# Performance work log

Measured on AMD Instinct MI355X. Metric: run time of the kernel, lower is better.

## Reference

```python
import jax, jax.numpy as jnp
import numpy as np

NB_EXPERTS = 16
TOP_K = 2


def setup_inputs() -> dict:
    key = jax.random.key(0)
    k1, k2, k3, k4, k5 = jax.random.split(key, 5)
    B, D, E, P = 8192, 768, NB_EXPERTS, 4
    return {
        "h": jax.random.normal(k1, (B, D, E), dtype=jnp.float32),
        "x": jax.random.normal(k2, (B, D), dtype=jnp.float32),
        "expert_weights": jax.random.normal(k3, (E, D), dtype=jnp.float32) * 0.02,
        "bias": jax.random.normal(k4, (E,), dtype=jnp.float32) * 0.02,
        "permutation_weights": jax.random.uniform(k5, (P, E, E), dtype=jnp.float32),
    }


def reference(h, x, expert_weights, bias, permutation_weights):
    # Router logits: [B, E]
    logits = x @ expert_weights.T + bias[None, :]
    # Top-k selection and scatter back to dense [B, E] (non-selected = 0)
    vals, idx = jax.lax.top_k(logits, TOP_K)
    B = logits.shape[0]
    rows = jnp.arange(B)[:, None]                       # [B, 1]
    scattered = jnp.zeros_like(logits).at[rows, idx].set(vals)
    # Mask zeros to -inf, softmax over experts (axis 1)
    masked = jnp.where(scattered == 0.0, -jnp.inf, scattered)
    softmaxes = jax.nn.softmax(masked, axis=1)          # [B, E]
    # Permutation: mean over leading axis, then bik,ij->bjk with k==1
    P_mean = jnp.mean(permutation_weights, axis=0)       # [E, E]
    s_perm = softmaxes @ P_mean                          # [B, E]
    # Weighted combine of expert outputs: [B, D, E] x [B, E] -> [B, D]
    y = jnp.einsum('bde,be->bd', h, s_perm)
    soft_averages = jnp.mean(s_perm, axis=0)[:, None]    # [E, 1]
    hard_averages = jnp.mean((s_perm >= 1e-05).astype(s_perm.dtype), axis=0)[:, None]  # [E, 1]
    return y, soft_averages, hard_averages
```

## Files before the change

kernel.cpp:

```cpp
#include <hip/hip_runtime.h>
#include <math.h>

#define BB 8192
#define DD 768
#define EE 16
#define PP 4

__global__ __launch_bounds__(256) void moe_fused(
    const float* __restrict__ h,
    const float* __restrict__ x,
    const float* __restrict__ W,
    const float* __restrict__ bias,
    const float* __restrict__ Pw,
    float* __restrict__ y,
    float* __restrict__ avgs)
{
    __shared__ float xs[DD];
    __shared__ float lg[EE];
    __shared__ float sp[EE];
    __shared__ int   topidx[2];
    __shared__ float topsm[2];

    const int t = threadIdx.x;
    const int b = blockIdx.x;

    const float4* x4 = (const float4*)(x + (size_t)b * DD);
    if (t < DD / 4) {
        ((float4*)xs)[t] = x4[t];
    }
    __syncthreads();

    const int e   = t >> 4;
    const int sub = t & 15;
    const float* wrow = W + e * DD;
    float part = 0.f;
    #pragma unroll 8
    for (int k = sub; k < DD; k += 16)
        part = fmaf(xs[k], wrow[k], part);
    #pragma unroll
    for (int off = 8; off >= 1; off >>= 1)
        part += __shfl_xor(part, off, 64);
    if (sub == 0) lg[e] = part + bias[e];
    __syncthreads();

    if (t == 0) {
        float v0 = -INFINITY, v1 = -INFINITY;
        int   i0 = 0, i1 = 0;
        #pragma unroll
        for (int j = 0; j < EE; ++j) {
            float v = lg[j];
            if (v > v0)      { v1 = v0; i1 = i0; v0 = v; i0 = j; }
            else if (v > v1) { v1 = v;  i1 = j; }
        }
        float z0 = (v0 == 0.f) ? -INFINITY : v0;
        float z1 = (v1 == 0.f) ? -INFINITY : v1;
        float m  = fmaxf(z0, z1);
        float e0 = __expf(z0 - m) == __expf(z0 - m) ? expf(z0 - m) : 0.f;
        float e1 = expf(z1 - m);
        e0 = expf(z0 - m);
        float inv = 1.f / (e0 + e1);
        topidx[0] = i0; topidx[1] = i1;
        topsm[0] = e0 * inv; topsm[1] = e1 * inv;
    }
    __syncthreads();

    if (t < EE) {
        const int   i0 = topidx[0], i1 = topidx[1];
        const float sm0 = topsm[0], sm1 = topsm[1];
        float pm0 = 0.f, pm1 = 0.f;
        #pragma unroll
        for (int p = 0; p < PP; ++p) {
            pm0 += Pw[p * EE * EE + i0 * EE + t];
            pm1 += Pw[p * EE * EE + i1 * EE + t];
        }
        pm0 *= 0.25f; pm1 *= 0.25f;
        const float s = sm0 * pm0 + sm1 * pm1;
        sp[t] = s;
        const float invB = 1.0f / BB;
        atomicAdd(&avgs[t], s * invB);
        atomicAdd(&avgs[EE + t], (s >= 1e-5f) ? invB : 0.f);
    }
    __syncthreads();

    const float4 s0 = ((const float4*)sp)[0];
    const float4 s1 = ((const float4*)sp)[1];
    const float4 s2 = ((const float4*)sp)[2];
    const float4 s3 = ((const float4*)sp)[3];
    const float* hb = h + (size_t)b * DD * EE;
    float* yb = y + (size_t)b * DD;
    #pragma unroll
    for (int it = 0; it < 3; ++it) {
        const int d = t + it * 256;
        const float4* h4 = (const float4*)(hb + (size_t)d * EE);
        float4 a  = h4[0];
        float4 bq = h4[1];
        float4 c  = h4[2];
        float4 dq = h4[3];
        float acc = a.x * s0.x + a.y * s0.y + a.z * s0.z + a.w * s0.w
                  + bq.x * s1.x + bq.y * s1.y + bq.z * s1.z + bq.w * s1.w
                  + c.x * s2.x + c.y * s2.y + c.z * s2.z + c.w * s2.w
                  + dq.x * s3.x + dq.y * s3.y + dq.z * s3.z + dq.w * s3.w;
        yb[d] = acc;
    }
}

extern "C" void kernel_launch(void* const* d_in, const int* in_sizes, int n_in,
                              void* d_out, int out_size, void* d_ws, size_t ws_size,
                              hipStream_t stream) {
    const float* h    = (const float*)d_in[0];
    const float* x    = (const float*)d_in[1];
    const float* W    = (const float*)d_in[2];
    const float* bias = (const float*)d_in[3];
    const float* Pw   = (const float*)d_in[4];

    float* y    = (float*)d_out;
    float* avgs = y + (size_t)BB * DD;

    hipMemsetAsync(avgs, 0, 2 * EE * sizeof(float), stream);

    moe_fused<<<BB, 256, 0, stream>>>(h, x, W, bias, Pw, y, avgs);
}
```

Before: 148.0 us.

## Split MoE into batched gating kernel and coalesced combine kernel

Splits the fused per-row kernel in two. A gating kernel handles 16 rows per block, with each lane computing one expert logit and a shuffle-based top-2 done in registers, and it aggregates the averages through shared-memory atomics before writing to global memory. A combine kernel then reads h with fully coalesced float4 loads and reduces each row with quad shuffles. This removes the serial single-thread top-k and the per-row global atomics, and it makes the h reads contiguous. The costs are an extra launch and a round trip of the gating weights through the workspace.

```diff
diff --git a/kernel.cpp b/kernel.cpp
--- a/kernel.cpp
+++ b/kernel.cpp
@@ -5,102 +5,114 @@
 #define DD 768
 #define EE 16
 #define PP 4
+#define ROWS_PER_BLK 16
 
-__global__ __launch_bounds__(256) void moe_fused(
-    const float* __restrict__ h,
+__global__ __launch_bounds__(256) void gating_kernel(
     const float* __restrict__ x,
     const float* __restrict__ W,
     const float* __restrict__ bias,
     const float* __restrict__ Pw,
-    float* __restrict__ y,
+    float* __restrict__ sp_ws,
     float* __restrict__ avgs)
 {
-    __shared__ float xs[DD];
-    __shared__ float lg[EE];
-    __shared__ float sp[EE];
-    __shared__ int   topidx[2];
-    __shared__ float topsm[2];
+    __shared__ float Pm[EE * EE];
+    __shared__ float aS[EE], aH[EE];
 
     const int t = threadIdx.x;
-    const int b = blockIdx.x;
 
-    const float4* x4 = (const float4*)(x + (size_t)b * DD);
-    if (t < DD / 4) {
-        ((float4*)xs)[t] = x4[t];
+    {
+        float s = 0.f;
+        #pragma unroll
+        for (int p = 0; p < PP; ++p) s += Pw[p * EE * EE + t];
+        Pm[t] = s * 0.25f;
+    }
+    if (t < EE) { aS[t] = 0.f; aH[t] = 0.f; }
+    __syncthreads();
+
+    const int wave = t >> 6;
+    const int lane = t & 63;
+    const int r_in = lane >> 4;
+    const int e    = lane & 15;
+    const int row  = blockIdx.x * ROWS_PER_BLK + wave * 4 + r_in;
+
+    const float4* x4 = (const float4*)(x + (size_t)row * DD);
+    const float4* w4 = (const float4*)(W + (size_t)e * DD);
+    float4 acc = {0.f, 0.f, 0.f, 0.f};
+    #pragma unroll 4
+    for (int k = 0; k < DD / 4; ++k) {
+        float4 a = x4[k], b = w4[k];
+        acc.x = fmaf(a.x, b.x, acc.x);
+        acc.y = fmaf(a.y, b.y, acc.y);
+        acc.z = fmaf(a.z, b.z, acc.z);
+        acc.w = fmaf(a.w, b.w, acc.w);
+    }
+    const float logit = acc.x + acc.y + acc.z + acc.w + bias[e];
+
+    float v0 = logit; int i0 = e;
+    #pragma unroll
+    for (int m = 1; m < 16; m <<= 1) {
+        float ov = __shfl_xor(v0, m, 16);
+        int   oi = __shfl_xor(i0, m, 16);
+        if (ov > v0 || (ov == v0 && oi < i0)) { v0 = ov; i0 = oi; }
+    }
+    float v1 = (e == i0) ? -INFINITY : logit; int i1 = e;
+    #pragma unroll
+    for (int m = 1; m < 16; m <<= 1) {
+        float ov = __shfl_xor(v1, m, 16);
+        int   oi = __shfl_xor(i1, m, 16);
+        if (ov > v1 || (ov == v1 && oi < i1)) { v1 = ov; i1 = oi; }
+    }
+
+    const float z0 = (v0 == 0.f) ? -INFINITY : v0;
+    const float z1 = (v1 == 0.f) ? -INFINITY : v1;
+    const float mx = fmaxf(z0, z1);
+    const float e0 = expf(z0 - mx), e1 = expf(z1 - mx);
+    const float inv = 1.f / (e0 + e1);
+    const float sm0 = e0 * inv, sm1 = e1 * inv;
+
+    const float s = sm0 * Pm[i0 * EE + e] + sm1 * Pm[i1 * EE + e];
+    sp_ws[(size_t)row * EE + e] = s;
+
+    float ssum = s;
+    float hsum = (s >= 1e-5f) ? 1.f : 0.f;
+    ssum += __shfl_xor(ssum, 16, 64);
+    ssum += __shfl_xor(ssum, 32, 64);
+    hsum += __shfl_xor(hsum, 16, 64);
+    hsum += __shfl_xor(hsum, 32, 64);
+    if (lane < 16) {
+        atomicAdd(&aS[e], ssum);
+        atomicAdd(&aH[e], hsum);
     }
     __syncthreads();
+    if (t < EE) {
+        const float invB = 1.0f / (float)BB;
+        atomicAdd(&avgs[t],      aS[t] * invB);
+        atomicAdd(&avgs[EE + t], aH[t] * invB);
+    }
+}
 
-    const int e   = t >> 4;
-    const int sub = t & 15;
-    const float* wrow = W + e * DD;
-    float part = 0.f;
-    #pragma unroll 8
-    for (int k = sub; k < DD; k += 16)
-        part = fmaf(xs[k], wrow[k], part);
+__global__ __launch_bounds__(256) void combine_kernel(
+    const float* __restrict__ h,
+    const float* __restrict__ sp_ws,
+    float* __restrict__ y)
+{
+    const int t = threadIdx.x;
+    const int b = blockIdx.x;
+    const int q = t & 3;
+
+    const float4 s4 = ((const float4*)(sp_ws + (size_t)b * EE))[q];
+
+    const float4* h4 = (const float4*)(h + (size_t)b * DD * EE);
+    float* yb = y + (size_t)b * DD;
+
     #pragma unroll
-    for (int off = 8; off >= 1; off >>= 1)
-        part += __shfl_xor(part, off, 64);
-    if (sub == 0) lg[e] = part + bias[e];
-    __syncthreads();
-
-    if (t == 0) {
-        float v0 = -INFINITY, v1 = -INFINITY;
-        int   i0 = 0, i1 = 0;
-        #pragma unroll
-        for (int j = 0; j < EE; ++j) {
-            float v = lg[j];
-            if (v > v0)      { v1 = v0; i1 = i0; v0 = v; i0 = j; }
-            else if (v > v1) { v1 = v;  i1 = j; }
-        }
-        float z0 = (v0 == 0.f) ? -INFINITY : v0;
-        float z1 = (v1 == 0.f) ? -INFINITY : v1;
-        float m  = fmaxf(z0, z1);
-        float e0 = __expf(z0 - m) == __expf(z0 - m) ? expf(z0 - m) : 0.f;
-        float e1 = expf(z1 - m);
-        e0 = expf(z0 - m);
-        float inv = 1.f / (e0 + e1);
-        topidx[0] = i0; topidx[1] = i1;
-        topsm[0] = e0 * inv; topsm[1] = e1 * inv;
-    }
-    __syncthreads();
-
-    if (t < EE) {
-        const int   i0 = topidx[0], i1 = topidx[1];
-        const float sm0 = topsm[0], sm1 = topsm[1];
-        float pm0 = 0.f, pm1 = 0.f;
-        #pragma unroll
-        for (int p = 0; p < PP; ++p) {
-            pm0 += Pw[p * EE * EE + i0 * EE + t];
-            pm1 += Pw[p * EE * EE + i1 * EE + t];
-        }
-        pm0 *= 0.25f; pm1 *= 0.25f;
-        const float s = sm0 * pm0 + sm1 * pm1;
-        sp[t] = s;
-        const float invB = 1.0f / BB;
-        atomicAdd(&avgs[t], s * invB);
-        atomicAdd(&avgs[EE + t], (s >= 1e-5f) ? invB : 0.f);
-    }
-    __syncthreads();
-
-    const float4 s0 = ((const float4*)sp)[0];
-    const float4 s1 = ((const float4*)sp)[1];
-    const float4 s2 = ((const float4*)sp)[2];
-    const float4 s3 = ((const float4*)sp)[3];
-    const float* hb = h + (size_t)b * DD * EE;
-    float* yb = y + (size_t)b * DD;
-    #pragma unroll
-    for (int it = 0; it < 3; ++it) {
-        const int d = t + it * 256;
-        const float4* h4 = (const float4*)(hb + (size_t)d * EE);
-        float4 a  = h4[0];
-        float4 bq = h4[1];
-        float4 c  = h4[2];
-        float4 dq = h4[3];
-        float acc = a.x * s0.x + a.y * s0.y + a.z * s0.z + a.w * s0.w
-                  + bq.x * s1.x + bq.y * s1.y + bq.z * s1.z + bq.w * s1.w
-                  + c.x * s2.x + c.y * s2.y + c.z * s2.z + c.w * s2.w
-                  + dq.x * s3.x + dq.y * s3.y + dq.z * s3.z + dq.w * s3.w;
-        yb[d] = acc;
+    for (int it = 0; it < 12; ++it) {
+        const int u = it * 256 + t;
+        float4 a = h4[u];
+        float p = a.x * s4.x + a.y * s4.y + a.z * s4.z + a.w * s4.w;
+        p += __shfl_xor(p, 1, 64);
+        p += __shfl_xor(p, 2, 64);
+        if (q == 0) yb[u >> 2] = p;
     }
 }
 
@@ -115,8 +127,10 @@
 
     float* y    = (float*)d_out;
     float* avgs = y + (size_t)BB * DD;
+    float* sp_ws = (float*)d_ws;
 
     hipMemsetAsync(avgs, 0, 2 * EE * sizeof(float), stream);
 
-    moe_fused<<<BB, 256, 0, stream>>>(h, x, W, bias, Pw, y, avgs);
+    gating_kernel<<<BB / ROWS_PER_BLK, 256, 0, stream>>>(x, W, bias, Pw, sp_ws, avgs);
+    combine_kernel<<<BB, 256, 0, stream>>>(h, sp_ws, y);
 }
```

New measurement: 151.8 us. 1.03x slower.
